# Kernel tuning notes

Hardware: AMD Instinct MI355X
Metric: run time of the kernel (lower is better)

## Reference

```python
import jax, jax.numpy as jnp
import numpy as np

DIM = 2048
NUM_HEADS = 16
HEAD_DIM = DIM // NUM_HEADS  # 128
B, L = 2, 2048


def setup_inputs() -> dict:
    key = jax.random.key(0)
    ks = jax.random.split(key, 5)
    x = jax.random.normal(ks[0], (B, L, DIM), dtype=jnp.float32)
    # genuine RoPE tables: inv_freq over half the head dim
    half = HEAD_DIM // 2
    inv_freq = 1.0 / (10000.0 ** (jnp.arange(half, dtype=jnp.float32) / half))
    ang = jnp.arange(L, dtype=jnp.float32)[:, None] * inv_freq[None, :]  # (L, half)
    cos = jnp.cos(ang)[:, None, :]  # (L, 1, half) broadcasts over (B,L,H,half)
    sin = jnp.sin(ang)[:, None, :]
    def dw_init(k, shape):
        fan_in, fan_out = shape
        std = 1.0 / np.sqrt(fan_in) * min(1.0, np.sqrt(fan_out / fan_in))
        return jax.random.normal(k, shape, dtype=jnp.float32) * std
    Wq = dw_init(ks[1], (DIM, DIM))
    Wk = dw_init(ks[2], (DIM, HEAD_DIM))
    Wv = dw_init(ks[3], (DIM, HEAD_DIM))
    Wo = dw_init(ks[4], (DIM, DIM))  # random instead of zeros so output is nontrivial
    return {"x": x, "cos": cos, "sin": sin, "Wq": Wq, "Wk": Wk, "Wv": Wv, "Wo": Wo}


def apply_rotary_emb(x, cos, sin):
    x1, x2 = jnp.split(x, 2, axis=-1)
    return jnp.concatenate([x1 * cos + x2 * sin, x1 * -sin + x2 * cos], axis=-1)


def rms_norm(x):
    return x * jax.lax.rsqrt(jnp.mean(x * x, axis=-1, keepdims=True) + 1e-6)


def reference(x, cos, sin, Wq, Wk, Wv, Wo):
    Bb, Ll, _ = x.shape
    q = (x @ Wq).reshape(Bb, Ll, NUM_HEADS, HEAD_DIM)  # (B,L,H,D)
    k = (x @ Wk)  # (B,L,D)  single KV head (MQA)
    v = (x @ Wv)  # (B,L,D)
    q = rms_norm(apply_rotary_emb(q, cos, sin))
    k = rms_norm(apply_rotary_emb(k[:, :, None, :], cos, sin))[:, :, 0, :]  # (B,L,D)
    scale = 1.0 / jnp.sqrt(jnp.asarray(HEAD_DIM, dtype=x.dtype))
    # scores without materializing broadcasted K: (B,H,Lq,Lk)
    scores = jnp.einsum('bqhd,bkd->bhqk', q, k) * scale
    causal = jnp.tril(jnp.ones((Ll, Ll), dtype=jnp.bool_))
    scores = jnp.where(causal[None, None], scores, jnp.asarray(-jnp.inf, dtype=scores.dtype))
    attn = jax.nn.softmax(scores, axis=-1)
    out = jnp.einsum('bhqk,bkd->bqhd', attn, v).reshape(Bb, Ll, DIM)
    return out @ Wo
```

## Files before the change

kernel.cpp:

```cpp
#include <hip/hip_runtime.h>

#define DIM 2048
#define NH 16
#define HD 128
#define BB 2
#define LL 2048
#define MROWS (BB * LL)
#define NKV 2304

typedef __attribute__((ext_vector_type(8))) short short8;
typedef __attribute__((ext_vector_type(4))) float floatx4;

__device__ inline ushort f2bf(float f) {
    union { float f; unsigned u; } v; v.f = f;
    unsigned r = v.u + 0x7FFFu + ((v.u >> 16) & 1u);
    return (ushort)(r >> 16);
}

#define GL16(g, l)                                                         \
    __builtin_amdgcn_global_load_lds(                                      \
        (const __attribute__((address_space(1))) unsigned int*)(g),        \
        (__attribute__((address_space(3))) unsigned int*)(l), 16, 0, 0)

__global__ __launch_bounds__(256) void conv_bf16(const float* __restrict__ in,
                                                 ushort* __restrict__ out) {
    size_t i = ((size_t)blockIdx.x * 256 + threadIdx.x) * 8;
    float4 a = *reinterpret_cast<const float4*>(in + i);
    float4 b = *reinterpret_cast<const float4*>(in + i + 4);
    ushort o[8] = {f2bf(a.x), f2bf(a.y), f2bf(a.z), f2bf(a.w),
                   f2bf(b.x), f2bf(b.y), f2bf(b.z), f2bf(b.w)};
    *reinterpret_cast<uint4*>(out + i) = *reinterpret_cast<uint4*>(o);
}

__global__ __launch_bounds__(256) void wprep(const float* __restrict__ Wq,
                                             const float* __restrict__ Wk,
                                             const float* __restrict__ Wv,
                                             const float* __restrict__ Wo,
                                             ushort* __restrict__ Wcatt,
                                             ushort* __restrict__ Wot) {
    __shared__ ushort T[64][72];
    const int bid = blockIdx.x;
    const float* in;
    ushort* out;
    int in_ld, c0, r0;
    const int out_ld = 2048;
    if (bid < 1024) {
        in = Wq; out = Wcatt; in_ld = 2048;
        c0 = (bid & 31) * 64; r0 = (bid >> 5) * 64;
    } else if (bid < 2048) {
        int t = bid - 1024;
        in = Wo; out = Wot; in_ld = 2048;
        c0 = (t & 31) * 64; r0 = (t >> 5) * 64;
    } else if (bid < 2112) {
        int t = bid - 2048;
        in = Wk; out = Wcatt + (size_t)2048 * 2048; in_ld = 128;
        c0 = (t & 1) * 64; r0 = (t >> 1) * 64;
    } else {
        int t = bid - 2112;
        in = Wv; out = Wcatt + (size_t)2176 * 2048; in_ld = 128;
        c0 = (t & 1) * 64; r0 = (t >> 1) * 64;
    }
    const int tid = threadIdx.x;
#pragma unroll
    for (int rep = 0; rep < 4; ++rep) {
        int idx = tid + rep * 256;
        int r = idx >> 4, c4 = idx & 15;
        float4 f = *reinterpret_cast<const float4*>(
            in + (size_t)(r0 + r) * in_ld + c0 + c4 * 4);
        T[r][c4 * 4 + 0] = f2bf(f.x);
        T[r][c4 * 4 + 1] = f2bf(f.y);
        T[r][c4 * 4 + 2] = f2bf(f.z);
        T[r][c4 * 4 + 3] = f2bf(f.w);
    }
    __syncthreads();
#pragma unroll
    for (int rep = 0; rep < 4; ++rep) {
        int idx = tid + rep * 256;
        int cr = idx >> 4, rc4 = idx & 15;
        uint a0 = (uint)T[rc4 * 4 + 0][cr] | ((uint)T[rc4 * 4 + 1][cr] << 16);
        uint a1 = (uint)T[rc4 * 4 + 2][cr] | ((uint)T[rc4 * 4 + 3][cr] << 16);
        uint2 val = {a0, a1};
        *reinterpret_cast<uint2*>(
            out + (size_t)(c0 + cr) * out_ld + r0 + rc4 * 4) = val;
    }
}

__global__ __launch_bounds__(256) void gemm_bf16(const ushort* __restrict__ A,
                                                 const ushort* __restrict__ Bt,
                                                 float* __restrict__ Y,
                                                 int K, int N) {
    __shared__ ushort As[128 * 64];
    __shared__ ushort Bs[128 * 64];
    const int tid = threadIdx.x;
    const int lane = tid & 63;
    const int w = tid >> 6;
    const int col = lane & 15, quad = lane >> 4;
    const int m0 = blockIdx.y * 128, n0 = blockIdx.x * 128;
    const int wm = (w >> 1) * 64, wn = (w & 1) * 64;

    floatx4 acc[4][4];
#pragma unroll
    for (int mt = 0; mt < 4; ++mt)
#pragma unroll
        for (int nt = 0; nt < 4; ++nt) acc[mt][nt] = (floatx4){0.f, 0.f, 0.f, 0.f};

    const int sr = tid >> 3;
    const int cg = (tid & 7) ^ (sr & 7);
    const int sel = col & 7;

    for (int k0 = 0; k0 < K; k0 += 64) {
        __syncthreads();
#pragma unroll
        for (int j = 0; j < 4; ++j)
            GL16(A + (size_t)(m0 + j * 32 + sr) * K + k0 + cg * 8,
                 As + (size_t)(j * 2048 + tid * 8));
#pragma unroll
        for (int j = 0; j < 4; ++j)
            GL16(Bt + (size_t)(n0 + j * 32 + sr) * K + k0 + cg * 8,
                 Bs + (size_t)(j * 2048 + tid * 8));
        __syncthreads();

#pragma unroll
        for (int kk = 0; kk < 2; ++kk) {
            short8 af[4], bf[4];
#pragma unroll
            for (int mt = 0; mt < 4; ++mt)
                af[mt] = *reinterpret_cast<const short8*>(
                    &As[(wm + mt * 16 + col) * 64 +
                        ((kk * 4 + quad) ^ sel) * 8]);
#pragma unroll
            for (int nt = 0; nt < 4; ++nt)
                bf[nt] = *reinterpret_cast<const short8*>(
                    &Bs[(wn + nt * 16 + col) * 64 +
                        ((kk * 4 + quad) ^ sel) * 8]);
#pragma unroll
            for (int mt = 0; mt < 4; ++mt)
#pragma unroll
                for (int nt = 0; nt < 4; ++nt)
                    acc[mt][nt] = __builtin_amdgcn_mfma_f32_16x16x32_bf16(
                        af[mt], bf[nt], acc[mt][nt], 0, 0, 0);
        }
    }

#pragma unroll
    for (int mt = 0; mt < 4; ++mt)
#pragma unroll
        for (int nt = 0; nt < 4; ++nt)
#pragma unroll
            for (int rr = 0; rr < 4; ++rr)
                Y[(size_t)(m0 + wm + mt * 16 + quad * 4 + rr) * N + n0 + wn +
                  nt * 16 + col] = acc[mt][nt][rr];
}

__global__ __launch_bounds__(256) void rope_rms_bf16(const float* __restrict__ in,
                                                     ushort* __restrict__ outb,
                                                     const float* __restrict__ cosb,
                                                     const float* __restrict__ sinb,
                                                     int heads, int nrows,
                                                     int in_ld) {
    int row = blockIdx.x * 4 + (threadIdx.x >> 6);
    int lane = threadIdx.x & 63;
    if (row >= nrows) return;
    int token = row / heads, head = row % heads;
    int l = token & (LL - 1);
    const float* p = in + (size_t)token * in_ld + head * HD;
    float x1 = p[lane];
    float x2 = p[lane + 64];
    float c = cosb[l * 64 + lane];
    float s = sinb[l * 64 + lane];
    float o1 = x1 * c + x2 * s;
    float o2 = -x1 * s + x2 * c;
    float ss = o1 * o1 + o2 * o2;
#pragma unroll
    for (int off = 32; off > 0; off >>= 1) ss += __shfl_xor(ss, off);
    float r = rsqrtf(ss * (1.0f / 128.0f) + 1e-6f);
    outb[(size_t)row * HD + lane] = f2bf(o1 * r);
    outb[(size_t)row * HD + lane + 64] = f2bf(o2 * r);
}

__global__ __launch_bounds__(256) void vtrans(const float* __restrict__ v,
                                              ushort* __restrict__ vt,
                                              int in_ld) {
    __shared__ ushort T[64][72];
    const int l0 = blockIdx.x * 64, d0 = blockIdx.y * 64, b = blockIdx.z;
    const int tid = threadIdx.x;
#pragma unroll
    for (int rep = 0; rep < 4; ++rep) {
        int idx = tid + rep * 256;
        int r = idx >> 4, c4 = idx & 15;
        float4 f = *reinterpret_cast<const float4*>(
            v + (size_t)(b * LL + l0 + r) * in_ld + d0 + c4 * 4);
        T[r][c4 * 4 + 0] = f2bf(f.x);
        T[r][c4 * 4 + 1] = f2bf(f.y);
        T[r][c4 * 4 + 2] = f2bf(f.z);
        T[r][c4 * 4 + 3] = f2bf(f.w);
    }
    __syncthreads();
#pragma unroll
    for (int rep = 0; rep < 4; ++rep) {
        int idx = tid + rep * 256;
        int dr = idx >> 4, lc4 = idx & 15;
        uint a0 = (uint)T[lc4 * 4 + 0][dr] | ((uint)T[lc4 * 4 + 1][dr] << 16);
        uint a1 = (uint)T[lc4 * 4 + 2][dr] | ((uint)T[lc4 * 4 + 3][dr] << 16);
        uint2 val = {a0, a1};
        *reinterpret_cast<uint2*>(
            vt + (size_t)(b * HD + d0 + dr) * LL + l0 + lc4 * 4) = val;
    }
}

__global__ __launch_bounds__(256) void flash_mfma(const ushort* __restrict__ qb,
                                                  const ushort* __restrict__ kb,
                                                  const ushort* __restrict__ vt,
                                                  ushort* __restrict__ aob) {
    __shared__ ushort Ks[64 * 128];
    __shared__ ushort VTs[128 * 64];
    __shared__ ushort Ps[4][16][72];

    const int tid = threadIdx.x;
    const int w = tid >> 6, lane = tid & 63;
    const int col = lane & 15, quad = lane >> 4;
    const int pairIdx = blockIdx.x, bh = blockIdx.y;
    const int b = bh >> 4, h = bh & 15;
    const int sel = col & 7;
    const float scl2 = 0.08838834764831845f * 1.44269504088896340736f;
    const float M2 = 11.5f * 1.44269504088896340736f;

    const int ksr[4] = {(tid + 0) >> 4, (tid + 256) >> 4, (tid + 512) >> 4,
                        (tid + 768) >> 4};
    const int vsr[4] = {(tid + 0) >> 3, (tid + 256) >> 3, (tid + 512) >> 3,
                        (tid + 768) >> 3};

    for (int sp = 0; sp < 2; ++sp) {
        const int qt = sp ? (31 - pairIdx) : pairIdx;
        const int q0 = qt * 64;

        const ushort* qrow =
            qb + ((size_t)(b * LL + q0 + w * 16 + col) * NH + h) * HD;
        short8 aq[4];
#pragma unroll
        for (int kc = 0; kc < 4; ++kc)
            aq[kc] = *reinterpret_cast<const short8*>(qrow + kc * 32 + quad * 8);

        float lrow[4] = {0.f, 0.f, 0.f, 0.f};
        floatx4 oacc[8];
#pragma unroll
        for (int dt = 0; dt < 8; ++dt) oacc[dt] = (floatx4){0.f, 0.f, 0.f, 0.f};

        const int ntiles = qt + 1;
        for (int kt = 0; kt < ntiles; ++kt) {
            const int k0 = kt * 64;
            __syncthreads();
#pragma unroll
            for (int rep = 0; rep < 4; ++rep) {
                int slot = tid + rep * 256;
                int r = ksr[rep];
                int gc = (slot & 15) ^ (r & 7);
                GL16(kb + (size_t)(b * LL + k0 + r) * HD + gc * 8,
                     Ks + (size_t)slot * 8);
            }
#pragma unroll
            for (int rep = 0; rep < 4; ++rep) {
                int slot = tid + rep * 256;
                int r = vsr[rep];
                int gc = (slot & 7) ^ (r & 7);
                GL16(vt + (size_t)(b * HD + r) * LL + k0 + gc * 8,
                     VTs + (size_t)slot * 8);
            }
            __syncthreads();

            floatx4 sacc[4];
#pragma unroll
            for (int nt = 0; nt < 4; ++nt)
                sacc[nt] = (floatx4){0.f, 0.f, 0.f, 0.f};
#pragma unroll
            for (int nt = 0; nt < 4; ++nt) {
#pragma unroll
                for (int kc = 0; kc < 4; ++kc) {
                    short8 bk = *reinterpret_cast<const short8*>(
                        &Ks[(nt * 16 + col) * 128 +
                            ((kc * 4 + quad) ^ sel) * 8]);
                    sacc[nt] = __builtin_amdgcn_mfma_f32_16x16x32_bf16(
                        aq[kc], bk, sacc[nt], 0, 0, 0);
                }
            }

            float psum[4] = {0.f, 0.f, 0.f, 0.f};
#pragma unroll
            for (int nt = 0; nt < 4; ++nt) {
                int kj = k0 + nt * 16 + col;
#pragma unroll
                for (int rr = 0; rr < 4; ++rr) {
                    int qi = q0 + w * 16 + quad * 4 + rr;
                    float p = exp2f(fmaf(sacc[nt][rr], scl2, -M2));
                    p = (kj <= qi) ? p : 0.0f;
                    sacc[nt][rr] = p;
                    psum[rr] += p;
                }
            }
#pragma unroll
            for (int rr = 0; rr < 4; ++rr) lrow[rr] += psum[rr];

#pragma unroll
            for (int nt = 0; nt < 4; ++nt)
#pragma unroll
                for (int rr = 0; rr < 4; ++rr)
                    Ps[w][quad * 4 + rr][nt * 16 + col] = f2bf(sacc[nt][rr]);
            asm volatile("s_waitcnt lgkmcnt(0)" ::: "memory");

#pragma unroll
            for (int kt2 = 0; kt2 < 2; ++kt2) {
                short8 ap = *reinterpret_cast<const short8*>(
                    &Ps[w][col][kt2 * 32 + quad * 8]);
#pragma unroll
                for (int dt = 0; dt < 8; ++dt) {
                    short8 bv = *reinterpret_cast<const short8*>(
                        &VTs[(dt * 16 + col) * 64 +
                             ((kt2 * 4 + quad) ^ sel) * 8]);
                    oacc[dt] = __builtin_amdgcn_mfma_f32_16x16x32_bf16(
                        ap, bv, oacc[dt], 0, 0, 0);
                }
            }
        }

#pragma unroll
        for (int off = 1; off < 16; off <<= 1)
#pragma unroll
            for (int rr = 0; rr < 4; ++rr)
                lrow[rr] += __shfl_xor(lrow[rr], off);
        float inv[4];
#pragma unroll
        for (int rr = 0; rr < 4; ++rr) inv[rr] = 1.0f / lrow[rr];
#pragma unroll
        for (int dt = 0; dt < 8; ++dt)
#pragma unroll
            for (int rr = 0; rr < 4; ++rr)
                aob[((size_t)(b * LL + q0 + w * 16 + quad * 4 + rr) * NH + h) *
                        HD + dt * 16 + col] = f2bf(oacc[dt][rr] * inv[rr]);
    }
}

extern "C" void kernel_launch(void* const* d_in, const int* in_sizes, int n_in,
                              void* d_out, int out_size, void* d_ws,
                              size_t ws_size, hipStream_t stream) {
    const float* x    = (const float*)d_in[0];
    const float* cosb = (const float*)d_in[1];
    const float* sinb = (const float*)d_in[2];
    const float* Wq   = (const float*)d_in[3];
    const float* Wk   = (const float*)d_in[4];
    const float* Wv   = (const float*)d_in[5];
    const float* Wo   = (const float*)d_in[6];
    float* out = (float*)d_out;

    float* qkv  = (float*)d_ws;
    ushort* xb  = (ushort*)(qkv + (size_t)MROWS * NKV);
    ushort* qb  = xb + (size_t)MROWS * DIM;
    ushort* kb  = qb + (size_t)MROWS * DIM;
    ushort* vt  = kb + (size_t)MROWS * HD;
    ushort* aob = vt + (size_t)MROWS * HD;
    ushort* Wcatt = aob + (size_t)MROWS * DIM;
    ushort* Wot   = Wcatt + (size_t)NKV * DIM;

    conv_bf16<<<dim3(MROWS * DIM / (256 * 8)), 256, 0, stream>>>(x, xb);
    wprep<<<dim3(2176), 256, 0, stream>>>(Wq, Wk, Wv, Wo, Wcatt, Wot);

    gemm_bf16<<<dim3(NKV / 128, MROWS / 128), 256, 0, stream>>>(xb, Wcatt, qkv,
                                                                DIM, NKV);

    rope_rms_bf16<<<dim3(MROWS * NH / 4), 256, 0, stream>>>(
        qkv, qb, cosb, sinb, NH, MROWS * NH, NKV);
    rope_rms_bf16<<<dim3(MROWS / 4), 256, 0, stream>>>(
        qkv + DIM, kb, cosb, sinb, 1, MROWS, NKV);
    vtrans<<<dim3(LL / 64, 2, BB), 256, 0, stream>>>(qkv + DIM + HD, vt, NKV);

    flash_mfma<<<dim3(LL / 128, BB * NH), 256, 0, stream>>>(qb, kb, vt, aob);

    gemm_bf16<<<dim3(DIM / 128, MROWS / 128), 256, 0, stream>>>(aob, Wot, out,
                                                                DIM, DIM);
}
```

Before: 326.6 us.

## Replace bf16 GEMM with 256x256 tile, 8-wave, double-buffered pipelined kernel

Swaps the 128x128 single-buffered GEMM for a 256x256 tile kernel with 512 threads and 8 waves. Global-to-LDS loads for future k-steps are staged in units interleaved with MFMA phases, using explicit waitcnt, barriers and setprio, so load latency overlaps compute. The larger tile gives more reuse per byte loaded, but it uses 128KB of LDS and produces fewer blocks: 9x16 for QKV and 8x16 for the output projection. K is hardcoded to 2048 via NT=32.

```diff
diff --git a/kernel.cpp b/kernel.cpp
--- a/kernel.cpp
+++ b/kernel.cpp
@@ -7,6 +7,7 @@
 #define LL 2048
 #define MROWS (BB * LL)
 #define NKV 2304
+#define NT 32
 
 typedef __attribute__((ext_vector_type(8))) short short8;
 typedef __attribute__((ext_vector_type(4))) float floatx4;
@@ -21,6 +22,10 @@
     __builtin_amdgcn_global_load_lds(                                      \
         (const __attribute__((address_space(1))) unsigned int*)(g),        \
         (__attribute__((address_space(3))) unsigned int*)(l), 16, 0, 0)
+
+__device__ __forceinline__ short8 ld8(const ushort* p) {
+    return *reinterpret_cast<const short8*>(p);
+}
 
 __global__ __launch_bounds__(256) void conv_bf16(const float* __restrict__ in,
                                                  ushort* __restrict__ out) {
@@ -85,71 +90,152 @@
     }
 }
 
-__global__ __launch_bounds__(256) void gemm_bf16(const ushort* __restrict__ A,
+template <int U>
+__device__ __forceinline__ void stage_unit(const ushort* __restrict__ A,
+                                           const ushort* __restrict__ Bt,
+                                           ushort* lbase, uint offA, uint offB,
+                                           int t) {
+    if (t >= NT) return;
+    const ushort* g = (U < 2) ? Bt : A;
+    uint off = ((U < 2) ? offB : offA) + ((U & 1) ? 128u * 2048u : 0u) +
+               (uint)t * 64u;
+    ushort* l = lbase + U * 8192;
+    GL16(g + off, l + (size_t)threadIdx.x * 8);
+    GL16(g + off + 64u * 2048u, l + (size_t)(threadIdx.x + 512) * 8);
+}
+
+__global__ __launch_bounds__(512, 2) void gemm8p(const ushort* __restrict__ A,
                                                  const ushort* __restrict__ Bt,
                                                  float* __restrict__ Y,
-                                                 int K, int N) {
-    __shared__ ushort As[128 * 64];
-    __shared__ ushort Bs[128 * 64];
+                                                 int N) {
+    __shared__ __attribute__((aligned(16))) ushort lds[65536];
     const int tid = threadIdx.x;
     const int lane = tid & 63;
     const int w = tid >> 6;
+    const int wm = w >> 2, wn = w & 3;
     const int col = lane & 15, quad = lane >> 4;
-    const int m0 = blockIdx.y * 128, n0 = blockIdx.x * 128;
-    const int wm = (w >> 1) * 64, wn = (w & 1) * 64;
-
-    floatx4 acc[4][4];
-#pragma unroll
-    for (int mt = 0; mt < 4; ++mt)
+    const int sel = col & 7;
+    const int m0 = blockIdx.y * 256, n0 = blockIdx.x * 256;
+
+    const int r0 = tid >> 3;
+    const int gc0 = (tid & 7) ^ (r0 & 7);
+    const uint offA = (uint)(m0 + r0) * 2048u + (uint)gc0 * 8u;
+    const uint offB = (uint)(n0 + r0) * 2048u + (uint)gc0 * 8u;
+
+    floatx4 acc[8][4];
+#pragma unroll
+    for (int mt = 0; mt < 8; ++mt)
 #pragma unroll
         for (int nt = 0; nt < 4; ++nt) acc[mt][nt] = (floatx4){0.f, 0.f, 0.f, 0.f};
 
-    const int sr = tid >> 3;
-    const int cg = (tid & 7) ^ (sr & 7);
-    const int sel = col & 7;
-
-    for (int k0 = 0; k0 < K; k0 += 64) {
-        __syncthreads();
-#pragma unroll
-        for (int j = 0; j < 4; ++j)
-            GL16(A + (size_t)(m0 + j * 32 + sr) * K + k0 + cg * 8,
-                 As + (size_t)(j * 2048 + tid * 8));
-#pragma unroll
-        for (int j = 0; j < 4; ++j)
-            GL16(Bt + (size_t)(n0 + j * 32 + sr) * K + k0 + cg * 8,
-                 Bs + (size_t)(j * 2048 + tid * 8));
-        __syncthreads();
-
-#pragma unroll
-        for (int kk = 0; kk < 2; ++kk) {
-            short8 af[4], bf[4];
-#pragma unroll
-            for (int mt = 0; mt < 4; ++mt)
-                af[mt] = *reinterpret_cast<const short8*>(
-                    &As[(wm + mt * 16 + col) * 64 +
-                        ((kk * 4 + quad) ^ sel) * 8]);
-#pragma unroll
-            for (int nt = 0; nt < 4; ++nt)
-                bf[nt] = *reinterpret_cast<const short8*>(
-                    &Bs[(wn + nt * 16 + col) * 64 +
-                        ((kk * 4 + quad) ^ sel) * 8]);
-#pragma unroll
-            for (int mt = 0; mt < 4; ++mt)
-#pragma unroll
-                for (int nt = 0; nt < 4; ++nt)
-                    acc[mt][nt] = __builtin_amdgcn_mfma_f32_16x16x32_bf16(
-                        af[mt], bf[nt], acc[mt][nt], 0, 0, 0);
-        }
-    }
-
-#pragma unroll
-    for (int mt = 0; mt < 4; ++mt)
+    const int aoff0 = (2 + wm) * 8192 + col * 64;
+    const int boff0 = (wn >> 1) * 8192 + ((wn & 1) * 64 + col) * 64;
+    const int koff0 = (quad ^ sel) * 8;
+    const int koff1 = ((4 + quad) ^ sel) * 8;
+
+    stage_unit<0>(A, Bt, lds, offA, offB, 0);
+    stage_unit<1>(A, Bt, lds, offA, offB, 0);
+    stage_unit<2>(A, Bt, lds, offA, offB, 0);
+    stage_unit<3>(A, Bt, lds, offA, offB, 0);
+    stage_unit<0>(A, Bt, lds + 32768, offA, offB, 1);
+    stage_unit<1>(A, Bt, lds + 32768, offA, offB, 1);
+    stage_unit<2>(A, Bt, lds + 32768, offA, offB, 1);
+    asm volatile("s_waitcnt vmcnt(6)" ::: "memory");
+    __builtin_amdgcn_s_barrier();
+
+#pragma unroll 2
+    for (int t = 0; t < NT; ++t) {
+        ushort* lb = lds + (t & 1) * 32768;
+        ushort* lbn = lds + ((t + 1) & 1) * 32768;
+
+        short8 a0[4], b0[4], b1[4];
+#pragma unroll
+        for (int mt = 0; mt < 4; ++mt)
+            a0[mt] = ld8(lb + aoff0 + mt * 16 * 64 + koff0);
 #pragma unroll
         for (int nt = 0; nt < 4; ++nt)
+            b0[nt] = ld8(lb + boff0 + nt * 16 * 64 + koff0);
+#pragma unroll
+        for (int nt = 0; nt < 4; ++nt)
+            b1[nt] = ld8(lb + boff0 + nt * 16 * 64 + koff1);
+        stage_unit<3>(A, Bt, lbn, offA, offB, t + 1);
+        __builtin_amdgcn_s_barrier();
+        asm volatile("s_waitcnt lgkmcnt(0)" ::: "memory");
+        __builtin_amdgcn_sched_barrier(0);
+        __builtin_amdgcn_s_setprio(1);
+#pragma unroll
+        for (int mt = 0; mt < 4; ++mt)
+#pragma unroll
+            for (int nt = 0; nt < 4; ++nt)
+                acc[mt][nt] = __builtin_amdgcn_mfma_f32_16x16x32_bf16(
+                    a0[mt], b0[nt], acc[mt][nt], 0, 0, 0);
+        __builtin_amdgcn_s_setprio(0);
+        __builtin_amdgcn_s_barrier();
+
+        short8 a1[4];
+#pragma unroll
+        for (int mt = 0; mt < 4; ++mt)
+            a1[mt] = ld8(lb + aoff0 + (4 + mt) * 16 * 64 + koff0);
+        stage_unit<0>(A, Bt, lb, offA, offB, t + 2);
+        __builtin_amdgcn_s_barrier();
+        asm volatile("s_waitcnt lgkmcnt(0)" ::: "memory");
+        __builtin_amdgcn_sched_barrier(0);
+        __builtin_amdgcn_s_setprio(1);
+#pragma unroll
+        for (int mt = 0; mt < 4; ++mt)
+#pragma unroll
+            for (int nt = 0; nt < 4; ++nt)
+                acc[4 + mt][nt] = __builtin_amdgcn_mfma_f32_16x16x32_bf16(
+                    a1[mt], b0[nt], acc[4 + mt][nt], 0, 0, 0);
+        __builtin_amdgcn_s_setprio(0);
+        __builtin_amdgcn_s_barrier();
+
+        short8 a2[4], a3[4];
+#pragma unroll
+        for (int mt = 0; mt < 4; ++mt)
+            a2[mt] = ld8(lb + aoff0 + mt * 16 * 64 + koff1);
+#pragma unroll
+        for (int mt = 0; mt < 4; ++mt)
+            a3[mt] = ld8(lb + aoff0 + (4 + mt) * 16 * 64 + koff1);
+        stage_unit<1>(A, Bt, lb, offA, offB, t + 2);
+        __builtin_amdgcn_s_barrier();
+        asm volatile("s_waitcnt lgkmcnt(0)" ::: "memory");
+        __builtin_amdgcn_sched_barrier(0);
+        __builtin_amdgcn_s_setprio(1);
+#pragma unroll
+        for (int mt = 0; mt < 4; ++mt)
+#pragma unroll
+            for (int nt = 0; nt < 4; ++nt)
+                acc[mt][nt] = __builtin_amdgcn_mfma_f32_16x16x32_bf16(
+                    a2[mt], b1[nt], acc[mt][nt], 0, 0, 0);
+        __builtin_amdgcn_s_setprio(0);
+        __builtin_amdgcn_s_barrier();
+
+        stage_unit<2>(A, Bt, lb, offA, offB, t + 2);
+        if (t < NT - 2)
+            asm volatile("s_waitcnt vmcnt(6)" ::: "memory");
+        else
+            asm volatile("s_waitcnt vmcnt(0)" ::: "memory");
+        __builtin_amdgcn_s_barrier();
+        __builtin_amdgcn_s_setprio(1);
+#pragma unroll
+        for (int mt = 0; mt < 4; ++mt)
+#pragma unroll
+            for (int nt = 0; nt < 4; ++nt)
+                acc[4 + mt][nt] = __builtin_amdgcn_mfma_f32_16x16x32_bf16(
+                    a3[mt], b1[nt], acc[4 + mt][nt], 0, 0, 0);
+        __builtin_amdgcn_s_setprio(0);
+        __builtin_amdgcn_s_barrier();
+    }
+
+#pragma unroll
+    for (int mt = 0; mt < 8; ++mt)
+#pragma unroll
+        for (int nt = 0; nt < 4; ++nt)
 #pragma unroll
             for (int rr = 0; rr < 4; ++rr)
-                Y[(size_t)(m0 + wm + mt * 16 + quad * 4 + rr) * N + n0 + wn +
-                  nt * 16 + col] = acc[mt][nt][rr];
+                Y[(size_t)(m0 + wm * 128 + mt * 16 + quad * 4 + rr) * N + n0 +
+                  wn * 64 + nt * 16 + col] = acc[mt][nt][rr];
 }
 
 __global__ __launch_bounds__(256) void rope_rms_bf16(const float* __restrict__ in,
@@ -363,8 +449,8 @@
     conv_bf16<<<dim3(MROWS * DIM / (256 * 8)), 256, 0, stream>>>(x, xb);
     wprep<<<dim3(2176), 256, 0, stream>>>(Wq, Wk, Wv, Wo, Wcatt, Wot);
 
-    gemm_bf16<<<dim3(NKV / 128, MROWS / 128), 256, 0, stream>>>(xb, Wcatt, qkv,
-                                                                DIM, NKV);
+    gemm8p<<<dim3(NKV / 256, MROWS / 256), 512, 0, stream>>>(xb, Wcatt, qkv,
+                                                             NKV);
 
     rope_rms_bf16<<<dim3(MROWS * NH / 4), 256, 0, stream>>>(
         qkv, qb, cosb, sinb, NH, MROWS * NH, NKV);
@@ -374,6 +460,6 @@
 
     flash_mfma<<<dim3(LL / 128, BB * NH), 256, 0, stream>>>(qb, kb, vt, aob);
 
-    gemm_bf16<<<dim3(DIM / 128, MROWS / 128), 256, 0, stream>>>(aob, Wot, out,
-                                                                DIM, DIM);
-}
+    gemm8p<<<dim3(DIM / 256, MROWS / 256), 512, 0, stream>>>(aob, Wot, out,
+                                                             DIM);
+}
```

Result: faster. 317.0 us (-2.9%).
